# Kernel tuning notes

Hardware: AMD Instinct MI355X
Metric: run time of the kernel (lower is better)

Reference implementation:

```python
import jax, jax.numpy as jnp
import numpy as np

USER_NUM = 500000
ITEM_NUM = 100000
D = 256        # embedding_size
MEM = 32       # memory_size
ATT = 256      # attention_size
B = 4096       # batch
NF = 64        # friends per user (padded with index == USER_NUM)


def _u(k, shape):
    return jax.random.uniform(k, shape, dtype=jnp.float32, minval=-0.1, maxval=0.1)


def setup_inputs() -> dict:
    key = jax.random.key(0)
    ks = jax.random.split(key, 12)
    return {
        "input_u": jax.random.randint(ks[0], (B,), 0, USER_NUM + 1),
        "input_i": jax.random.randint(ks[1], (B,), 0, ITEM_NUM),
        "input_uf": jax.random.randint(ks[2], (B, NF), 0, USER_NUM + 1),
        "uidW": _u(ks[3], (USER_NUM + 1, D)),
        "iidW": _u(ks[4], (ITEM_NUM, D)),
        "i_bias": jnp.zeros((ITEM_NUM,), jnp.float32),
        "Key": _u(ks[5], (D, MEM)),
        "Mem": jnp.ones((MEM, D), jnp.float32),
        "WA": _u(ks[6], (D, ATT)),
        "BA": jnp.zeros((ATT,), jnp.float32),
        "U_omega": _u(ks[7], (ATT, 1)),
        "att_exp1": jax.random.normal(ks[8], (2 * D, 2), jnp.float32) * 0.05,
    }


def _l2norm(x, axis):
    # torch F.normalize(p=2): x / max(||x||, eps)
    n = jnp.sqrt(jnp.sum(x * x, axis=axis, keepdims=True))
    return x / jnp.maximum(n, 1e-12)


def reference(input_u, input_i, input_uf, uidW, iidW, i_bias, Key, Mem, WA, BA, U_omega, att_exp1):
    uid = uidW[input_u]                        # [B, D]
    iid = iidW[input_i]                        # [B, D]
    i_b = i_bias[input_i]                      # [B]
    fe = uidW[input_uf]                        # [B, F, D]
    frien_num = (input_uf != USER_NUM).astype(jnp.float32)  # [B, F] valid mask
    fe = frien_num[:, :, None] * fe

    uid_n = _l2norm(uid, axis=1)
    fe_n = _l2norm(fe, axis=2)
    cross = uid_n[:, None, :] * fe_n           # [B, F, D]

    att_key = jnp.einsum('bfd,dm->bfm', cross, Key)          # [B, F, M]
    att_mem = jax.nn.softmax(att_key, axis=0)                # NOTE: softmax over BATCH dim (faithful)
    att_mem = frien_num[:, :, None] * att_mem

    f1 = jnp.einsum('bfm,md->bfd', att_mem, Mem)             # [B, F, D]
    f2 = f1 * fe                                             # [B, F, D]

    h = jax.nn.relu(jnp.einsum('bfd,da->bfa', f2, WA) + BA)  # [B, F, A]
    j = jnp.exp(jnp.einsum('bfa,ao->bfo', h, U_omega))       # [B, F, 1]
    j = frien_num[:, :, None] * j
    w = j / (jnp.sum(j, axis=1, keepdims=True) + 1e-8)       # [B, F, 1]
    friend = jnp.sum(w * f2, axis=1)                         # [B, D]
    # dropout(p=dp) in eval mode -> identity

    user = uid + friend
    att1 = jax.nn.softmax(jnp.concatenate([uid, user], axis=1) @ att_exp1, axis=1)  # [B, 2]
    user_f = uid * att1[:, 0:1] + user * att1[:, 1:2]
    score = jnp.sum(user_f * iid, axis=1) + i_b              # [B]
    return score
```

## Files before the change

kernel.cpp:

```cpp
#include <hip/hip_runtime.h>

#define USER_NUM 500000
#define BATCH 4096
#define NF 64
#define DIM 256
#define MEMN 32
#define ATTN 256

typedef short bf16x8 __attribute__((ext_vector_type(8)));
typedef float f32x4 __attribute__((ext_vector_type(4)));

__device__ __forceinline__ unsigned short f2bf(float f) {
    unsigned u = __float_as_uint(f);
    u += 0x7FFFu + ((u >> 16) & 1u);
    return (unsigned short)(u >> 16);
}
__device__ __forceinline__ float bf2f(unsigned short s) {
    return __uint_as_float(((unsigned)s) << 16);
}
__device__ __forceinline__ bf16x8 as_frag(uint4 v) {
    return __builtin_bit_cast(bf16x8, v);
}

__device__ __forceinline__ float block_reduce_sum(float v, float* scr) {
#pragma unroll
    for (int o = 32; o; o >>= 1) v += __shfl_xor(v, o, 64);
    __syncthreads();
    if ((threadIdx.x & 63) == 0) scr[threadIdx.x >> 6] = v;
    __syncthreads();
    return scr[0] + scr[1] + scr[2] + scr[3];
}

__device__ __forceinline__ float2 block_reduce_sum2(float a, float b, float* scr) {
#pragma unroll
    for (int o = 32; o; o >>= 1) {
        a += __shfl_xor(a, o, 64);
        b += __shfl_xor(b, o, 64);
    }
    __syncthreads();
    if ((threadIdx.x & 63) == 0) {
        scr[(threadIdx.x >> 6) * 2]     = a;
        scr[(threadIdx.x >> 6) * 2 + 1] = b;
    }
    __syncthreads();
    float2 r;
    r.x = scr[0] + scr[2] + scr[4] + scr[6];
    r.y = scr[1] + scr[3] + scr[5] + scr[7];
    return r;
}

#define WS_AK    0u
#define WS_FE    33554432u
#define WS_KEYT  167772160u
#define WS_MEMT  167788544u
#define WS_WATT  167804928u
#define WS_PART  167936000u
#define WS_SSUM  168001536u

__global__ __launch_bounds__(256) void kprep(const float* __restrict__ Key,
                                             unsigned short* __restrict__ keyT) {
    int gid = blockIdx.x * 256 + threadIdx.x;
    int m = gid >> 8, d = gid & 255;
    keyT[gid] = f2bf(Key[d * 32 + m]);
}

__global__ __launch_bounds__(256, 4) void katt(const int* __restrict__ input_u,
                                               const int* __restrict__ input_uf,
                                               const float* __restrict__ uidW,
                                               const unsigned short* __restrict__ keyT_ws,
                                               unsigned short* __restrict__ fe_ws,
                                               float* __restrict__ ak) {
    extern __shared__ char smem[];
    float* uidn = (float*)(smem + 33792);
    float* scr  = (float*)(smem + 34816);
    const int b = blockIdx.x, t = threadIdx.x;
    const int w = t >> 6, l = t & 63, q = l >> 4;

    int iu   = input_u[b];
    int myuf = input_uf[b * NF + w * 16 + (l & 15)];
    float uv = uidW[(size_t)iu * DIM + t];

    float4 fe[16];
#pragma unroll
    for (int i = 0; i < 16; i++) {
        int idx = __shfl(myuf, i, 64);
        fe[i] = ((const float4*)(uidW + (size_t)idx * DIM))[l];
    }

    float ss = block_reduce_sum(uv * uv, scr);
    float inv = 1.0f / fmaxf(sqrtf(ss), 1e-12f);
    uidn[t] = uv * inv;
    __syncthreads();

    float4 un4 = *(const float4*)(uidn + l * 4);
#pragma unroll
    for (int i = 0; i < 16; i++) {
        int f = w * 16 + i;
        float mk = (__shfl(myuf, i, 64) != USER_NUM) ? 1.0f : 0.0f;
        float x = fe[i].x * mk, y = fe[i].y * mk, z = fe[i].z * mk, ww = fe[i].w * mk;
        float s2 = x * x + y * y + z * z + ww * ww;
#pragma unroll
        for (int o = 32; o; o >>= 1) s2 += __shfl_xor(s2, o, 64);
        float rn = 1.0f / fmaxf(sqrtf(s2), 1e-12f);
        ushort4 fb;
        fb.x = f2bf(x); fb.y = f2bf(y); fb.z = f2bf(z); fb.w = f2bf(ww);
        *(ushort4*)(fe_ws + (size_t)b * 16384 + f * 256 + l * 4) = fb;
        ushort4 o4;
        o4.x = f2bf(un4.x * x * rn);
        o4.y = f2bf(un4.y * y * rn);
        o4.z = f2bf(un4.z * z * rn);
        o4.w = f2bf(un4.w * ww * rn);
        *(ushort4*)(smem + f * 528 + l * 8) = o4;
    }
    __syncthreads();

    const uint4* kp = (const uint4*)keyT_ws;
    f32x4 acc0 = {0.f, 0.f, 0.f, 0.f}, acc1 = {0.f, 0.f, 0.f, 0.f};
#pragma unroll
    for (int kt = 0; kt < 8; kt++) {
        bf16x8 aF = *(const bf16x8*)(smem + (w * 16 + (l & 15)) * 528 + kt * 64 + q * 16);
        bf16x8 b0 = as_frag(kp[(l & 15) * 32 + kt * 4 + q]);
        bf16x8 b1 = as_frag(kp[((l & 15) + 16) * 32 + kt * 4 + q]);
        acc0 = __builtin_amdgcn_mfma_f32_16x16x32_bf16(aF, b0, acc0, 0, 0, 0);
        acc1 = __builtin_amdgcn_mfma_f32_16x16x32_bf16(aF, b1, acc1, 0, 0, 0);
    }
    {
        int fbase = w * 16 + q * 4;
        int m = l & 15;
#pragma unroll
        for (int r = 0; r < 4; r++) {
            ak[((size_t)b * NF + fbase + r) * MEMN + m]      = __expf(acc0[r]);
            ak[((size_t)b * NF + fbase + r) * MEMN + 16 + m] = __expf(acc1[r]);
        }
    }
}

__global__ __launch_bounds__(256) void ksum1(const float* __restrict__ ak, float* __restrict__ part) {
    __shared__ float pl[256];
    int bid = blockIdx.x;
    int f = bid >> 3, c = bid & 7;
    int t = threadIdx.x, m = t & 31, g = t >> 5;
    float s = 0.f;
    size_t base = ((size_t)(c * 512 + g) * NF + f) * MEMN + m;
#pragma unroll 8
    for (int i = 0; i < 64; i++) {
        s += ak[base];
        base += (size_t)8 * NF * MEMN;
    }
    pl[t] = s;
    __syncthreads();
    if (t < 32) {
        float tot = 0.f;
#pragma unroll
        for (int gg = 0; gg < 8; gg++) tot += pl[gg * 32 + t];
        part[c * 2048 + f * 32 + t] = tot;
    }
}
__global__ __launch_bounds__(256) void ksum2(const float* __restrict__ part,
                                             float* __restrict__ ssum,
                                             const float* __restrict__ Mem,
                                             const float* __restrict__ WA,
                                             unsigned short* __restrict__ memT,
                                             unsigned short* __restrict__ watt) {
    int fm = blockIdx.x * 256 + threadIdx.x;
    float s = 0.f;
#pragma unroll
    for (int c = 0; c < 8; c++) s += part[c * 2048 + fm];
    ssum[fm] = 1.0f / s;
    for (int e = fm; e < 8192; e += 2048) {
        int d = e >> 5, m = e & 31;
        memT[e] = f2bf(Mem[m * 256 + d]);
    }
    for (int e = fm; e < 65536; e += 2048) {
        int kt = e >> 13, r = e & 8191, a = r >> 5, kk = r & 31;
        watt[e] = f2bf(WA[(kt * 32 + kk) * 256 + a]);
    }
}

#define OFF_AM   33792
#define OFF_JP   38912
#define OFF_W    39936
#define OFF_SCR  40704
__global__ __launch_bounds__(256, 3) void kmain(const int* __restrict__ input_u,
                                                const int* __restrict__ input_i,
                                                const int* __restrict__ input_uf,
                                                const float* __restrict__ uidW,
                                                const float* __restrict__ iidW,
                                                const float* __restrict__ i_bias,
                                                const float* __restrict__ BA,
                                                const float* __restrict__ U_omega,
                                                const float* __restrict__ att_exp1,
                                                const float* __restrict__ ak,
                                                const float* __restrict__ ssum_ws,
                                                const unsigned short* __restrict__ fe_ws,
                                                const unsigned short* __restrict__ memT_ws,
                                                const unsigned short* __restrict__ watt_ws,
                                                float* __restrict__ out) {
    extern __shared__ char smem[];
    float* jpL  = (float*)(smem + OFF_JP);
    float* wL   = (float*)(smem + OFF_W);
    float* scr  = (float*)(smem + OFF_SCR);
    const int b = blockIdx.x, t = threadIdx.x;
    const int w = t >> 6, l = t & 63, q = l >> 4;

    int iu = input_u[b], ii = input_i[b];
    float uidv = uidW[(size_t)iu * DIM + t];
    float iidv = iidW[(size_t)ii * DIM + t];
    float ib   = i_bias[ii];
    float ae00 = att_exp1[t * 2], ae01 = att_exp1[t * 2 + 1];
    float ae10 = att_exp1[(DIM + t) * 2], ae11 = att_exp1[(DIM + t) * 2 + 1];
    int uf_f = input_uf[b * NF + (t >> 2)];
    int uf_t = input_uf[b * NF + (t & 63)];
    const float4* akp = (const float4*)(ak + (size_t)b * 2048);
    const float4* rp  = (const float4*)ssum_ws;
    float4 a0 = akp[2 * t], a1 = akp[2 * t + 1];
    float4 r0 = rp[2 * t],  r1 = rp[2 * t + 1];
    ushort4 feb[16];
#pragma unroll
    for (int i = 0; i < 16; i++)
        feb[i] = *(const ushort4*)(fe_ws + (size_t)b * 16384 + (w * 16 + i) * 256 + l * 4);

    {
        float mk = (uf_f != USER_NUM) ? 1.0f : 0.0f;
        float v0 = mk * a0.x * r0.x;
        float v1 = mk * a0.y * r0.y;
        float v2 = mk * a0.z * r0.z;
        float v3 = mk * a0.w * r0.w;
        float v4 = mk * a1.x * r1.x;
        float v5 = mk * a1.y * r1.y;
        float v6 = mk * a1.z * r1.z;
        float v7 = mk * a1.w * r1.w;
        uint4 pk;
        pk.x = (unsigned)f2bf(v0) | ((unsigned)f2bf(v1) << 16);
        pk.y = (unsigned)f2bf(v2) | ((unsigned)f2bf(v3) << 16);
        pk.z = (unsigned)f2bf(v4) | ((unsigned)f2bf(v5) << 16);
        pk.w = (unsigned)f2bf(v6) | ((unsigned)f2bf(v7) << 16);
        *(uint4*)(smem + OFF_AM + (t >> 2) * 80 + (t & 3) * 16) = pk;
    }
    __syncthreads();

    {
        const uint4* mp = (const uint4*)memT_ws;
        bf16x8 aF[4];
#pragma unroll
        for (int ft = 0; ft < 4; ft++)
            aF[ft] = *(const bf16x8*)(smem + OFF_AM + (ft * 16 + (l & 15)) * 80 + q * 16);
#pragma unroll
        for (int dti = 0; dti < 4; dti++) {
            int dt = 4 * w + dti;
            bf16x8 bF = as_frag(mp[(dt * 16 + (l & 15)) * 4 + q]);
            int dcol = dt * 16 + (l & 15);
#pragma unroll
            for (int ft = 0; ft < 4; ft++) {
                f32x4 acc = {0.f, 0.f, 0.f, 0.f};
                acc = __builtin_amdgcn_mfma_f32_16x16x32_bf16(aF[ft], bF, acc, 0, 0, 0);
                int fbase = ft * 16 + q * 4;
#pragma unroll
                for (int r = 0; r < 4; r++)
                    *(unsigned short*)(smem + (fbase + r) * 528 + dcol * 2) = f2bf(acc[r]);
            }
        }
    }
    __syncthreads();

    {
#pragma unroll
        for (int i = 0; i < 16; i++) {
            int f = w * 16 + i;
            ushort4* p = (ushort4*)(smem + f * 528 + l * 8);
            ushort4 fv = *p;
            ushort4 o4;
            o4.x = f2bf(bf2f(fv.x) * bf2f(feb[i].x));
            o4.y = f2bf(bf2f(fv.y) * bf2f(feb[i].y));
            o4.z = f2bf(bf2f(fv.z) * bf2f(feb[i].z));
            o4.w = f2bf(bf2f(fv.w) * bf2f(feb[i].w));
            *p = o4;
        }
    }
    __syncthreads();

    f32x4 acc[4][4];
    {
        f32x4 z = {0.f, 0.f, 0.f, 0.f};
#pragma unroll
        for (int ft = 0; ft < 4; ft++)
#pragma unroll
            for (int at = 0; at < 4; at++) acc[ft][at] = z;
    }
    {
        const uint4* wp = (const uint4*)watt_ws;
        for (int kt = 0; kt < 8; kt++) {
            bf16x8 aF[4], bF[4];
#pragma unroll
            for (int ft = 0; ft < 4; ft++)
                aF[ft] = *(const bf16x8*)(smem + (ft * 16 + (l & 15)) * 528 + kt * 64 + q * 16);
#pragma unroll
            for (int at = 0; at < 4; at++)
                bF[at] = as_frag(wp[kt * 1024 + (64 * w + at * 16 + (l & 15)) * 4 + q]);
#pragma unroll
            for (int ft = 0; ft < 4; ft++)
#pragma unroll
                for (int at = 0; at < 4; at++)
                    acc[ft][at] = __builtin_amdgcn_mfma_f32_16x16x32_bf16(aF[ft], bF[at], acc[ft][at], 0, 0, 0);
        }
    }
    {
        float jp[16];
#pragma unroll
        for (int i = 0; i < 16; i++) jp[i] = 0.f;
#pragma unroll
        for (int at = 0; at < 4; at++) {
            int a = 64 * w + at * 16 + (l & 15);
            float ba = BA[a], uw = U_omega[a];
#pragma unroll
            for (int ft = 0; ft < 4; ft++)
#pragma unroll
                for (int r = 0; r < 4; r++) {
                    float h = fmaxf(acc[ft][at][r] + ba, 0.f);
                    jp[ft * 4 + r] += h * uw;
                }
        }
#pragma unroll
        for (int mask = 1; mask < 16; mask <<= 1)
#pragma unroll
            for (int i = 0; i < 16; i++) jp[i] += __shfl_xor(jp[i], mask, 64);
        if ((l & 15) == 0) {
#pragma unroll
            for (int ft = 0; ft < 4; ft++)
#pragma unroll
                for (int r = 0; r < 4; r++)
                    jpL[w * 64 + ft * 16 + q * 4 + r] = jp[ft * 4 + r];
        }
    }
    __syncthreads();

    if (t < 64) {
        float logit = jpL[t] + jpL[64 + t] + jpL[128 + t] + jpL[192 + t];
        float jv = ((uf_t != USER_NUM) ? 1.0f : 0.0f) * __expf(logit);
        float s = jv;
#pragma unroll
        for (int o = 32; o; o >>= 1) s += __shfl_xor(s, o, 64);
        wL[t] = jv / (s + 1e-8f);
    }
    __syncthreads();

    float fr = 0.f;
#pragma unroll 8
    for (int f = 0; f < 64; f++)
        fr += wL[f] * bf2f(*(unsigned short*)(smem + f * 528 + t * 2));

    float user = uidv + fr;
    float2 ll = block_reduce_sum2(uidv * ae00 + user * ae10, uidv * ae01 + user * ae11, scr);
    float mx = fmaxf(ll.x, ll.y);
    float e0 = __expf(ll.x - mx), e1 = __expf(ll.y - mx);
    float rinv = 1.0f / (e0 + e1);
    float a0w = e0 * rinv, a1w = e1 * rinv;
    float sc = block_reduce_sum((uidv * a0w + user * a1w) * iidv, scr);
    if (t == 0) out[b] = sc + ib;
}

extern "C" void kernel_launch(void* const* d_in, const int* in_sizes, int n_in,
                              void* d_out, int out_size, void* d_ws, size_t ws_size,
                              hipStream_t stream) {
    const int*   input_u  = (const int*)d_in[0];
    const int*   input_i  = (const int*)d_in[1];
    const int*   input_uf = (const int*)d_in[2];
    const float* uidW     = (const float*)d_in[3];
    const float* iidW     = (const float*)d_in[4];
    const float* i_bias   = (const float*)d_in[5];
    const float* Key      = (const float*)d_in[6];
    const float* Mem      = (const float*)d_in[7];
    const float* WA       = (const float*)d_in[8];
    const float* BA       = (const float*)d_in[9];
    const float* U_omega  = (const float*)d_in[10];
    const float* att_exp1 = (const float*)d_in[11];
    float* out = (float*)d_out;
    char* ws = (char*)d_ws;

    float*          ak   = (float*)(ws + WS_AK);
    unsigned short* fe   = (unsigned short*)(ws + WS_FE);
    unsigned short* keyT = (unsigned short*)(ws + WS_KEYT);
    unsigned short* memT = (unsigned short*)(ws + WS_MEMT);
    unsigned short* watt = (unsigned short*)(ws + WS_WATT);
    float*          part = (float*)(ws + WS_PART);
    float*          ssum = (float*)(ws + WS_SSUM);

    hipLaunchKernelGGL(kprep, dim3(32), dim3(256), 0, stream, Key, keyT);
    hipLaunchKernelGGL(katt, dim3(BATCH), dim3(256), 34880, stream, input_u, input_uf, uidW, keyT, fe, ak);
    hipLaunchKernelGGL(ksum1, dim3(512), dim3(256), 0, stream, ak, part);
    hipLaunchKernelGGL(ksum2, dim3(8), dim3(256), 0, stream, part, ssum, Mem, WA, memT, watt);
    hipLaunchKernelGGL(kmain, dim3(BATCH), dim3(256), 40768, stream, input_u, input_i, input_uf,
                       uidW, iidW, i_bias, BA, U_omega, att_exp1, ak, ssum, fe, memT, watt, out);
}
```

Baseline: 791.3 us.

## Store attention exponentials in bf16, merge prep kernels, use atomics for batch softmax sums

The exp(att_key) buffer is stored as bf16 instead of fp32, halving its write and its two reads. The ksum2 kernel is removed: the Mem and WA transposes move into kprep, and the batch-softmax column sums are accumulated with atomicAdd into a zeroed buffer, with the reciprocal taken in kmain. In katt the user norm is reduced per wave without LDS or barriers, and the friend-row loads are split into two software-pipelined halves to cut register use. In kmain the final weights are broadcast with shuffles instead of LDS plus a barrier. The risks are lower precision in the softmax numerators and sums, and atomic contention on 2048 addresses.

```diff
diff --git a/kernel.cpp b/kernel.cpp
--- a/kernel.cpp
+++ b/kernel.cpp
@@ -22,15 +22,6 @@
     return __builtin_bit_cast(bf16x8, v);
 }
 
-__device__ __forceinline__ float block_reduce_sum(float v, float* scr) {
-#pragma unroll
-    for (int o = 32; o; o >>= 1) v += __shfl_xor(v, o, 64);
-    __syncthreads();
-    if ((threadIdx.x & 63) == 0) scr[threadIdx.x >> 6] = v;
-    __syncthreads();
-    return scr[0] + scr[1] + scr[2] + scr[3];
-}
-
 __device__ __forceinline__ float2 block_reduce_sum2(float a, float b, float* scr) {
 #pragma unroll
     for (int o = 32; o; o >>= 1) {
@@ -47,6 +38,14 @@
     r.x = scr[0] + scr[2] + scr[4] + scr[6];
     r.y = scr[1] + scr[3] + scr[5] + scr[7];
     return r;
+}
+__device__ __forceinline__ float block_reduce_sum(float v, float* scr) {
+#pragma unroll
+    for (int o = 32; o; o >>= 1) v += __shfl_xor(v, o, 64);
+    __syncthreads();
+    if ((threadIdx.x & 63) == 0) scr[threadIdx.x >> 6] = v;
+    __syncthreads();
+    return scr[0] + scr[1] + scr[2] + scr[3];
 }
 
 #define WS_AK    0u
@@ -54,14 +53,29 @@
 #define WS_KEYT  167772160u
 #define WS_MEMT  167788544u
 #define WS_WATT  167804928u
-#define WS_PART  167936000u
 #define WS_SSUM  168001536u
 
 __global__ __launch_bounds__(256) void kprep(const float* __restrict__ Key,
-                                             unsigned short* __restrict__ keyT) {
+                                             const float* __restrict__ Mem,
+                                             const float* __restrict__ WA,
+                                             unsigned short* __restrict__ keyT,
+                                             unsigned short* __restrict__ memT,
+                                             unsigned short* __restrict__ watt,
+                                             float* __restrict__ ssum) {
     int gid = blockIdx.x * 256 + threadIdx.x;
-    int m = gid >> 8, d = gid & 255;
-    keyT[gid] = f2bf(Key[d * 32 + m]);
+    if (gid < 8192) {
+        int m = gid >> 8, d = gid & 255;
+        keyT[gid] = f2bf(Key[d * 32 + m]);
+    } else if (gid < 16384) {
+        int e = gid - 8192, d = e >> 5, m = e & 31;
+        memT[e] = f2bf(Mem[m * 256 + d]);
+    } else if (gid < 81920) {
+        int e = gid - 16384;
+        int kt = e >> 13, r = e & 8191, a = r >> 5, kk = r & 31;
+        watt[e] = f2bf(WA[(kt * 32 + kk) * 256 + a]);
+    } else {
+        ssum[gid - 81920] = 0.f;
+    }
 }
 
 __global__ __launch_bounds__(256, 4) void katt(const int* __restrict__ input_u,
@@ -69,35 +83,42 @@
                                                const float* __restrict__ uidW,
                                                const unsigned short* __restrict__ keyT_ws,
                                                unsigned short* __restrict__ fe_ws,
-                                               float* __restrict__ ak) {
+                                               unsigned short* __restrict__ ak) {
     extern __shared__ char smem[];
-    float* uidn = (float*)(smem + 33792);
-    float* scr  = (float*)(smem + 34816);
     const int b = blockIdx.x, t = threadIdx.x;
     const int w = t >> 6, l = t & 63, q = l >> 4;
 
     int iu   = input_u[b];
     int myuf = input_uf[b * NF + w * 16 + (l & 15)];
-    float uv = uidW[(size_t)iu * DIM + t];
-
-    float4 fe[16];
+    float4 u4 = ((const float4*)(uidW + (size_t)iu * DIM))[l];
+
+    float4 fv[8];
+#pragma unroll
+    for (int i = 0; i < 8; i++) {
+        int idx = __shfl(myuf, i, 64);
+        fv[i] = ((const float4*)(uidW + (size_t)idx * DIM))[l];
+    }
+
+    float ssp = u4.x * u4.x + u4.y * u4.y + u4.z * u4.z + u4.w * u4.w;
+#pragma unroll
+    for (int o = 32; o; o >>= 1) ssp += __shfl_xor(ssp, o, 64);
+    float inv = 1.0f / fmaxf(sqrtf(ssp), 1e-12f);
+    float4 un4;
+    un4.x = u4.x * inv; un4.y = u4.y * inv; un4.z = u4.z * inv; un4.w = u4.w * inv;
+
+    float4 fv2[8];
 #pragma unroll
     for (int i = 0; i < 16; i++) {
-        int idx = __shfl(myuf, i, 64);
-        fe[i] = ((const float4*)(uidW + (size_t)idx * DIM))[l];
-    }
-
-    float ss = block_reduce_sum(uv * uv, scr);
-    float inv = 1.0f / fmaxf(sqrtf(ss), 1e-12f);
-    uidn[t] = uv * inv;
-    __syncthreads();
-
-    float4 un4 = *(const float4*)(uidn + l * 4);
-#pragma unroll
-    for (int i = 0; i < 16; i++) {
+        if (i < 8) {
+            int idx2 = __shfl(myuf, i + 8, 64);
+            fv2[i] = ((const float4*)(uidW + (size_t)idx2 * DIM))[l];
+        }
+        float4 cur;
+        if (i < 8) cur = fv[i]; else cur = fv2[i - 8];
         int f = w * 16 + i;
-        float mk = (__shfl(myuf, i, 64) != USER_NUM) ? 1.0f : 0.0f;
-        float x = fe[i].x * mk, y = fe[i].y * mk, z = fe[i].z * mk, ww = fe[i].w * mk;
+        int idc = __shfl(myuf, i, 64);
+        float mk = (idc != USER_NUM) ? 1.0f : 0.0f;
+        float x = cur.x * mk, y = cur.y * mk, z = cur.z * mk, ww = cur.w * mk;
         float s2 = x * x + y * y + z * z + ww * ww;
 #pragma unroll
         for (int o = 32; o; o >>= 1) s2 += __shfl_xor(s2, o, 64);
@@ -129,13 +150,14 @@
         int m = l & 15;
 #pragma unroll
         for (int r = 0; r < 4; r++) {
-            ak[((size_t)b * NF + fbase + r) * MEMN + m]      = __expf(acc0[r]);
-            ak[((size_t)b * NF + fbase + r) * MEMN + 16 + m] = __expf(acc1[r]);
-        }
-    }
-}
-
-__global__ __launch_bounds__(256) void ksum1(const float* __restrict__ ak, float* __restrict__ part) {
+            unsigned short* row = ak + ((size_t)b * NF + fbase + r) * MEMN;
+            row[m]      = f2bf(__expf(acc0[r]));
+            row[m + 16] = f2bf(__expf(acc1[r]));
+        }
+    }
+}
+
+__global__ __launch_bounds__(256) void ksum1(const unsigned short* __restrict__ ak, float* __restrict__ ssum) {
     __shared__ float pl[256];
     int bid = blockIdx.x;
     int f = bid >> 3, c = bid & 7;
@@ -144,7 +166,7 @@
     size_t base = ((size_t)(c * 512 + g) * NF + f) * MEMN + m;
 #pragma unroll 8
     for (int i = 0; i < 64; i++) {
-        s += ak[base];
+        s += bf2f(ak[base]);
         base += (size_t)8 * NF * MEMN;
     }
     pl[t] = s;
@@ -153,34 +175,13 @@
         float tot = 0.f;
 #pragma unroll
         for (int gg = 0; gg < 8; gg++) tot += pl[gg * 32 + t];
-        part[c * 2048 + f * 32 + t] = tot;
-    }
-}
-__global__ __launch_bounds__(256) void ksum2(const float* __restrict__ part,
-                                             float* __restrict__ ssum,
-                                             const float* __restrict__ Mem,
-                                             const float* __restrict__ WA,
-                                             unsigned short* __restrict__ memT,
-                                             unsigned short* __restrict__ watt) {
-    int fm = blockIdx.x * 256 + threadIdx.x;
-    float s = 0.f;
-#pragma unroll
-    for (int c = 0; c < 8; c++) s += part[c * 2048 + fm];
-    ssum[fm] = 1.0f / s;
-    for (int e = fm; e < 8192; e += 2048) {
-        int d = e >> 5, m = e & 31;
-        memT[e] = f2bf(Mem[m * 256 + d]);
-    }
-    for (int e = fm; e < 65536; e += 2048) {
-        int kt = e >> 13, r = e & 8191, a = r >> 5, kk = r & 31;
-        watt[e] = f2bf(WA[(kt * 32 + kk) * 256 + a]);
+        atomicAdd(&ssum[f * 32 + t], tot);
     }
 }
 
 #define OFF_AM   33792
 #define OFF_JP   38912
-#define OFF_W    39936
-#define OFF_SCR  40704
+#define OFF_SCR  39936
 __global__ __launch_bounds__(256, 3) void kmain(const int* __restrict__ input_u,
                                                 const int* __restrict__ input_i,
                                                 const int* __restrict__ input_uf,
@@ -190,7 +191,7 @@
                                                 const float* __restrict__ BA,
                                                 const float* __restrict__ U_omega,
                                                 const float* __restrict__ att_exp1,
-                                                const float* __restrict__ ak,
+                                                const unsigned short* __restrict__ ak,
                                                 const float* __restrict__ ssum_ws,
                                                 const unsigned short* __restrict__ fe_ws,
                                                 const unsigned short* __restrict__ memT_ws,
@@ -198,7 +199,6 @@
                                                 float* __restrict__ out) {
     extern __shared__ char smem[];
     float* jpL  = (float*)(smem + OFF_JP);
-    float* wL   = (float*)(smem + OFF_W);
     float* scr  = (float*)(smem + OFF_SCR);
     const int b = blockIdx.x, t = threadIdx.x;
     const int w = t >> 6, l = t & 63, q = l >> 4;
@@ -211,10 +211,10 @@
     float ae10 = att_exp1[(DIM + t) * 2], ae11 = att_exp1[(DIM + t) * 2 + 1];
     int uf_f = input_uf[b * NF + (t >> 2)];
     int uf_t = input_uf[b * NF + (t & 63)];
-    const float4* akp = (const float4*)(ak + (size_t)b * 2048);
-    const float4* rp  = (const float4*)ssum_ws;
-    float4 a0 = akp[2 * t], a1 = akp[2 * t + 1];
-    float4 r0 = rp[2 * t],  r1 = rp[2 * t + 1];
+    const uint4* akp = (const uint4*)(ak + (size_t)b * 2048);
+    uint4 av = akp[t];
+    const float4* sp = (const float4*)ssum_ws;
+    float4 s0 = sp[2 * t], s1 = sp[2 * t + 1];
     ushort4 feb[16];
 #pragma unroll
     for (int i = 0; i < 16; i++)
@@ -222,14 +222,14 @@
 
     {
         float mk = (uf_f != USER_NUM) ? 1.0f : 0.0f;
-        float v0 = mk * a0.x * r0.x;
-        float v1 = mk * a0.y * r0.y;
-        float v2 = mk * a0.z * r0.z;
-        float v3 = mk * a0.w * r0.w;
-        float v4 = mk * a1.x * r1.x;
-        float v5 = mk * a1.y * r1.y;
-        float v6 = mk * a1.z * r1.z;
-        float v7 = mk * a1.w * r1.w;
+        float v0 = mk * bf2f((unsigned short)(av.x & 0xffff)) * __builtin_amdgcn_rcpf(s0.x);
+        float v1 = mk * bf2f((unsigned short)(av.x >> 16))    * __builtin_amdgcn_rcpf(s0.y);
+        float v2 = mk * bf2f((unsigned short)(av.y & 0xffff)) * __builtin_amdgcn_rcpf(s0.z);
+        float v3 = mk * bf2f((unsigned short)(av.y >> 16))    * __builtin_amdgcn_rcpf(s0.w);
+        float v4 = mk * bf2f((unsigned short)(av.z & 0xffff)) * __builtin_amdgcn_rcpf(s1.x);
+        float v5 = mk * bf2f((unsigned short)(av.z >> 16))    * __builtin_amdgcn_rcpf(s1.y);
+        float v6 = mk * bf2f((unsigned short)(av.w & 0xffff)) * __builtin_amdgcn_rcpf(s1.z);
+        float v7 = mk * bf2f((unsigned short)(av.w >> 16))    * __builtin_amdgcn_rcpf(s1.w);
         uint4 pk;
         pk.x = (unsigned)f2bf(v0) | ((unsigned)f2bf(v1) << 16);
         pk.y = (unsigned)f2bf(v2) | ((unsigned)f2bf(v3) << 16);
@@ -334,20 +334,19 @@
     }
     __syncthreads();
 
-    if (t < 64) {
-        float logit = jpL[t] + jpL[64 + t] + jpL[128 + t] + jpL[192 + t];
+    float fr;
+    {
+        float logit = jpL[l] + jpL[64 + l] + jpL[128 + l] + jpL[192 + l];
         float jv = ((uf_t != USER_NUM) ? 1.0f : 0.0f) * __expf(logit);
-        float s = jv;
-#pragma unroll
-        for (int o = 32; o; o >>= 1) s += __shfl_xor(s, o, 64);
-        wL[t] = jv / (s + 1e-8f);
-    }
-    __syncthreads();
-
-    float fr = 0.f;
+        float sj = jv;
+#pragma unroll
+        for (int o = 32; o; o >>= 1) sj += __shfl_xor(sj, o, 64);
+        float wv = jv / (sj + 1e-8f);
+        fr = 0.f;
 #pragma unroll 8
-    for (int f = 0; f < 64; f++)
-        fr += wL[f] * bf2f(*(unsigned short*)(smem + f * 528 + t * 2));
+        for (int f = 0; f < 64; f++)
+            fr += __shfl(wv, f, 64) * bf2f(*(unsigned short*)(smem + f * 528 + t * 2));
+    }
 
     float user = uidv + fr;
     float2 ll = block_reduce_sum2(uidv * ae00 + user * ae10, uidv * ae01 + user * ae11, scr);
@@ -377,18 +376,16 @@
     float* out = (float*)d_out;
     char* ws = (char*)d_ws;
 
-    float*          ak   = (float*)(ws + WS_AK);
+    unsigned short* ak   = (unsigned short*)(ws + WS_AK);
     unsigned short* fe   = (unsigned short*)(ws + WS_FE);
     unsigned short* keyT = (unsigned short*)(ws + WS_KEYT);
     unsigned short* memT = (unsigned short*)(ws + WS_MEMT);
     unsigned short* watt = (unsigned short*)(ws + WS_WATT);
-    float*          part = (float*)(ws + WS_PART);
     float*          ssum = (float*)(ws + WS_SSUM);
 
-    hipLaunchKernelGGL(kprep, dim3(32), dim3(256), 0, stream, Key, keyT);
-    hipLaunchKernelGGL(katt, dim3(BATCH), dim3(256), 34880, stream, input_u, input_uf, uidW, keyT, fe, ak);
-    hipLaunchKernelGGL(ksum1, dim3(512), dim3(256), 0, stream, ak, part);
-    hipLaunchKernelGGL(ksum2, dim3(8), dim3(256), 0, stream, part, ssum, Mem, WA, memT, watt);
-    hipLaunchKernelGGL(kmain, dim3(BATCH), dim3(256), 40768, stream, input_u, input_i, input_uf,
+    hipLaunchKernelGGL(kprep, dim3(328), dim3(256), 0, stream, Key, Mem, WA, keyT, memT, watt, ssum);
+    hipLaunchKernelGGL(katt, dim3(BATCH), dim3(256), 33792, stream, input_u, input_uf, uidW, keyT, fe, ak);
+    hipLaunchKernelGGL(ksum1, dim3(512), dim3(256), 0, stream, ak, ssum);
+    hipLaunchKernelGGL(kmain, dim3(BATCH), dim3(256), 40000, stream, input_u, input_i, input_uf,
                        uidW, iidW, i_bias, BA, U_omega, att_exp1, ak, ssum, fe, memT, watt, out);
 }
```

Measured after the change: 771.3 us. 2.5% less time.
